# Optimization experiments

Measured on AMD Instinct MI355X. Metric: run time of the kernel, lower is better.

The kernel has to match this reference:

```python
import jax, jax.numpy as jnp
import numpy as np

N = 100000
E = 1600000
NFEAT = 256
NCLASS = 40
H1, C1 = 8, 8  # layer1: 8 heads x 8 channels, concat -> 64
EPS = 1e-16
NEG_SLOPE = 0.2


def setup_inputs() -> dict:
    key = jax.random.key(0)
    ks = jax.random.split(key, 10)
    x = jax.random.normal(ks[0], (N, NFEAT), dtype=jnp.float32)
    # random edges with no self-loops (PyG GATConv removes then re-adds self loops)
    src = jax.random.randint(ks[1], (E,), 0, N)
    off = jax.random.randint(ks[2], (E,), 1, N)
    dst = (src + off) % N
    edge_index = jnp.stack([src, dst]).astype(jnp.int64)
    glorot = lambda k, shp, fan: jax.random.uniform(k, shp, jnp.float32, -1.0, 1.0) * np.sqrt(6.0 / fan)
    # layer 1: in=256 -> heads=8, out=8
    W1 = glorot(ks[3], (NFEAT, H1 * C1), NFEAT + H1 * C1)
    att_src1 = glorot(ks[4], (H1, C1), 2 * C1)
    att_dst1 = glorot(ks[5], (H1, C1), 2 * C1)
    b1 = jnp.zeros((H1 * C1,), jnp.float32)
    # layer 2: in=64 -> heads=1, out=nclass
    W2 = glorot(ks[6], (H1 * C1, NCLASS), H1 * C1 + NCLASS)
    att_src2 = glorot(ks[7], (1, NCLASS), 2 * NCLASS)
    att_dst2 = glorot(ks[8], (1, NCLASS), 2 * NCLASS)
    b2 = jnp.zeros((NCLASS,), jnp.float32)
    return {"x": x, "edge_index": edge_index, "W1": W1, "att_src1": att_src1,
            "att_dst1": att_dst1, "b1": b1, "W2": W2, "att_src2": att_src2,
            "att_dst2": att_dst2, "b2": b2}


def gat_conv(x, src, dst, W, att_src, att_dst, bias, heads, out_ch):
    n = x.shape[0]
    h = (x @ W).reshape(n, heads, out_ch)               # [N,H,C]
    a_src = (h * att_src[None]).sum(-1)                  # [N,H]
    a_dst = (h * att_dst[None]).sum(-1)                  # [N,H]
    e = jax.nn.leaky_relu(a_src[src] + a_dst[dst], NEG_SLOPE)  # [E,H]
    # segment softmax over incoming edges of each target node
    m = jax.ops.segment_max(e, dst, num_segments=n)
    e = jnp.exp(e - m[dst])
    s = jax.ops.segment_sum(e, dst, num_segments=n)
    alpha = e / (s[dst] + EPS)                           # [E,H]
    msg = h[src] * alpha[..., None]                      # [E,H,C]
    out = jax.ops.segment_sum(msg, dst, num_segments=n)  # [N,H,C]
    return out.reshape(n, heads * out_ch) + bias


def reference(x, edge_index, W1, att_src1, att_dst1, b1, W2, att_src2, att_dst2, b2):
    # add self loops (PyG GATConv default add_self_loops=True)
    loops = jnp.arange(N, dtype=edge_index.dtype)
    src = jnp.concatenate([edge_index[0], loops])
    dst = jnp.concatenate([edge_index[1], loops])
    h = gat_conv(x, src, dst, W1, att_src1, att_dst1, b1, H1, C1)  # [N,64]
    h = jax.nn.elu(h)
    out = gat_conv(h, src, dst, W2, att_src2, att_dst2, b2, 1, NCLASS)  # [N,nclass]
    return out
```

## Files before the change

### kernel.cpp

```cpp
#include <hip/hip_runtime.h>
#include <hip/hip_bf16.h>

#define NN 100000
#define NE 1600000
#define NF 256
#define NC 40
#define NH 8
#define D1 64
#define NEG 0.2f
#define BSHIFT 7
#define BSZ 128
#define NB ((NN + BSZ - 1) / BSZ)
#define EPB 4096
#define NBLK ((NE + EPB - 1) / EPB)

typedef __attribute__((ext_vector_type(8))) short short8;
typedef __attribute__((ext_vector_type(4))) float f32x4;

static __device__ __forceinline__ float lrelu(float x) { return x > 0.f ? x : NEG * x; }

static __device__ __forceinline__ float2 bfx2(unsigned u) {
    union { unsigned q; float f; } a, b;
    a.q = u << 16;
    b.q = u & 0xFFFF0000u;
    return make_float2(a.f, b.f);
}

static __device__ __forceinline__ unsigned packbf2(float x, float y) {
    unsigned xu = __float_as_uint(x), yu = __float_as_uint(y);
    xu = (xu + 0x7FFFu + ((xu >> 16) & 1u)) >> 16;
    yu = (yu + 0x7FFFu + ((yu >> 16) & 1u)) >> 16;
    return xu | (yu << 16);
}

static __device__ __forceinline__ unsigned short f2b(float x) {
    unsigned u = __float_as_uint(x);
    u = (u + 0x7FFFu + ((u >> 16) & 1u)) >> 16;
    return (unsigned short)u;
}


__launch_bounds__(256)
__global__ void bhist_k(const int* __restrict__ dst, int* __restrict__ cnt) {
    __shared__ int hist[NB];
    int i = blockIdx.x, t = threadIdx.x;
    for (int b = t; b < NB; b += 256) hist[b] = 0;
    __syncthreads();
    int e0 = i * EPB;
    #pragma unroll
    for (int k = 0; k < EPB / 256; ++k) {
        int e = e0 + k * 256 + t;
        if (e < NE) atomicAdd(&hist[dst[e] >> BSHIFT], 1);
    }
    __syncthreads();
    for (int b = t; b < NB; b += 256) cnt[i * NB + b] = hist[b];
}

__launch_bounds__(256)
__global__ void bscan2_k(int* __restrict__ cnt, int* __restrict__ btot) {
    __shared__ int ps[256];
    int b = blockIdx.x, t = threadIdx.x;
    int i0 = 2 * t;
    int a = (i0 < NBLK) ? cnt[i0 * NB + b] : 0;
    int c = (i0 + 1 < NBLK) ? cnt[(i0 + 1) * NB + b] : 0;
    int s = a + c;
    ps[t] = s;
    __syncthreads();
    #pragma unroll
    for (int off = 1; off < 256; off <<= 1) {
        int x = (t >= off) ? ps[t - off] : 0;
        __syncthreads();
        ps[t] += x;
        __syncthreads();
    }
    int ex = ps[t] - s;
    if (i0 < NBLK) cnt[i0 * NB + b] = ex;
    if (i0 + 1 < NBLK) cnt[(i0 + 1) * NB + b] = ex + a;
    if (t == 255) btot[b] = ps[255];
}

__launch_bounds__(256)
__global__ void bscanB_k(const int* __restrict__ btot, int* __restrict__ bbase) {
    __shared__ int ps[256];
    int t = threadIdx.x;
    int j0 = 4 * t;
    int v[4]; int s = 0;
    #pragma unroll
    for (int k = 0; k < 4; ++k) { v[k] = (j0 + k < NB) ? btot[j0 + k] : 0; s += v[k]; }
    ps[t] = s;
    __syncthreads();
    #pragma unroll
    for (int off = 1; off < 256; off <<= 1) {
        int x = (t >= off) ? ps[t - off] : 0;
        __syncthreads();
        ps[t] += x;
        __syncthreads();
    }
    int run = ps[t] - s;
    #pragma unroll
    for (int k = 0; k < 4; ++k) { if (j0 + k < NB) bbase[j0 + k] = run; run += v[k]; }
    if (t == 0) bbase[NB] = NE;
}

__launch_bounds__(256)
__global__ void bplace_k(const int* __restrict__ src, const int* __restrict__ dst,
                         const int* __restrict__ cnt, const int* __restrict__ bbase,
                         long long* __restrict__ tmp) {
    __shared__ int loff[NB];
    int i = blockIdx.x, t = threadIdx.x;
    for (int b = t; b < NB; b += 256) loff[b] = bbase[b] + cnt[i * NB + b];
    __syncthreads();
    int e0 = i * EPB;
    #pragma unroll
    for (int k = 0; k < EPB / 256; ++k) {
        int e = e0 + k * 256 + t;
        if (e < NE) {
            int d = dst[e];
            int p = atomicAdd(&loff[d >> BSHIFT], 1);
            tmp[p] = ((long long)d << 32) | (unsigned)src[e];
        }
    }
}

__launch_bounds__(256)
__global__ void scatter2_k(const long long* __restrict__ tmp, const int* __restrict__ bbase,
                           int* __restrict__ rowptr, int* __restrict__ col) {
    __shared__ int lcnt[BSZ];
    __shared__ int lrow[BSZ];
    __shared__ int ls[BSZ];
    int b = blockIdx.x, t = threadIdx.x;
    int n0 = b << BSHIFT;
    if (t < BSZ) lcnt[t] = 0;
    __syncthreads();
    int beg = bbase[b], end = bbase[b + 1];
    for (int p = beg + t; p < end; p += 256) {
        int d = (int)(tmp[p] >> 32);
        atomicAdd(&lcnt[d - n0], 1);
    }
    __syncthreads();
    if (t < BSZ) ls[t] = lcnt[t];
    __syncthreads();
    #pragma unroll
    for (int off = 1; off < BSZ; off <<= 1) {
        int x = 0;
        if (t < BSZ && t >= off) x = ls[t - off];
        __syncthreads();
        if (t < BSZ) ls[t] += x;
        __syncthreads();
    }
    if (t < BSZ) {
        int ex = ls[t] - lcnt[t];
        lrow[t] = beg + ex;
        if (n0 + t < NN) rowptr[n0 + t] = beg + ex;
        lcnt[t] = 0;
    }
    if (b == NB - 1 && t == 0) rowptr[NN] = NE;
    __syncthreads();
    for (int p = beg + t; p < end; p += 256) {
        long long v = tmp[p];
        int d = (int)(v >> 32);
        int s = (int)(v & 0xFFFFFFFFLL);
        int o = atomicAdd(&lcnt[d - n0], 1);
        col[lrow[d - n0] + o] = s;
    }
}


__launch_bounds__(256)
__global__ void gemm1_k(const float* __restrict__ x, const float* __restrict__ W,
                        unsigned short* __restrict__ h1b) {
    __shared__ unsigned short wsw[8 * 4 * 64 * 8];
    int tid = threadIdx.x;
    int wid = tid >> 6, lane = tid & 63;
    int r0 = blockIdx.x * 128 + wid * 32;

    #pragma unroll
    for (int it = 0; it < 16; ++it) {
        int idx4 = it * 256 + tid;
        int k = idx4 >> 4;
        int c0 = (idx4 & 15) * 4;
        float4 v = *(const float4*)&W[k * 64 + c0];
        int kt = k >> 5, kg = (k >> 3) & 3, kr = k & 7;
        float vv[4] = {v.x, v.y, v.z, v.w};
        #pragma unroll
        for (int j = 0; j < 4; ++j) {
            int c = c0 + j;
            int dest = (((kt * 4 + (c >> 4)) * 64) + kg * 16 + (c & 15)) * 8 + kr;
            wsw[dest] = f2b(vv[j]);
        }
    }
    __syncthreads();

    int arow0 = r0 + (lane & 15);
    int kg8 = (lane >> 4) * 8;
    f32x4 acc[2][4] = {};
    for (int kt = 0; kt < 8; ++kt) {
        short8 af[2];
        #pragma unroll
        for (int rt = 0; rt < 2; ++rt) {
            int row = arow0 + rt * 16;
            float4 v0 = make_float4(0.f, 0.f, 0.f, 0.f), v1 = v0;
            if (row < NN) {
                const float* px = &x[row * NF + kt * 32 + kg8];
                v0 = *(const float4*)px;
                v1 = *(const float4*)(px + 4);
            }
            unsigned p0 = packbf2(v0.x, v0.y), p1 = packbf2(v0.z, v0.w);
            unsigned p2 = packbf2(v1.x, v1.y), p3 = packbf2(v1.z, v1.w);
            af[rt][0] = (short)(p0 & 0xFFFF); af[rt][1] = (short)(p0 >> 16);
            af[rt][2] = (short)(p1 & 0xFFFF); af[rt][3] = (short)(p1 >> 16);
            af[rt][4] = (short)(p2 & 0xFFFF); af[rt][5] = (short)(p2 >> 16);
            af[rt][6] = (short)(p3 & 0xFFFF); af[rt][7] = (short)(p3 >> 16);
        }
        #pragma unroll
        for (int ct = 0; ct < 4; ++ct) {
            short8 bf = *(const short8*)&wsw[((kt * 4 + ct) * 64 + lane) * 8];
            acc[0][ct] = __builtin_amdgcn_mfma_f32_16x16x32_bf16(af[0], bf, acc[0][ct], 0, 0, 0);
            acc[1][ct] = __builtin_amdgcn_mfma_f32_16x16x32_bf16(af[1], bf, acc[1][ct], 0, 0, 0);
        }
    }

    int ccol = lane & 15;
    int crow0 = r0 + (lane >> 4) * 4;
    #pragma unroll
    for (int rt = 0; rt < 2; ++rt) {
        #pragma unroll
        for (int r = 0; r < 4; ++r) {
            int grow = crow0 + rt * 16 + r;
            if (grow < NN) {
                #pragma unroll
                for (int ct = 0; ct < 4; ++ct)
                    h1b[grow * D1 + ct * 16 + ccol] = f2b(acc[rt][ct][r]);
            }
        }
    }
}


__global__ void attn1_k(const unsigned short* __restrict__ h1b, const float* __restrict__ asrc,
                        const float* __restrict__ adst,
                        float* __restrict__ as1, float* __restrict__ ad1) {
    int t = blockIdx.x * blockDim.x + threadIdx.x;
    if (t >= NN * NH) return;
    int n = t >> 3, h = t & 7;
    uint4 v = *(const uint4*)&h1b[n * D1 + h * 8];
    float hv[8];
    float2 p;
    p = bfx2(v.x); hv[0] = p.x; hv[1] = p.y;
    p = bfx2(v.y); hv[2] = p.x; hv[3] = p.y;
    p = bfx2(v.z); hv[4] = p.x; hv[5] = p.y;
    p = bfx2(v.w); hv[6] = p.x; hv[7] = p.y;
    float sa = 0.f, sd = 0.f;
    #pragma unroll
    for (int c = 0; c < 8; ++c) {
        sa = fmaf(hv[c], asrc[h * 8 + c], sa);
        sd = fmaf(hv[c], adst[h * 8 + c], sd);
    }
    as1[t] = sa;
    ad1[t] = sd;
}


__launch_bounds__(256)
__global__ void agg1_k(const unsigned short* __restrict__ h1b, const float* __restrict__ as1,
                       const float* __restrict__ ad1,
                       const int* __restrict__ rowptr, const int* __restrict__ col,
                       const float* __restrict__ b1, unsigned short* __restrict__ h1outb) {
    int n = blockIdx.x * 4 + (threadIdx.x >> 6);
    if (n >= NN) return;
    int lane = threadIdx.x & 63;
    int g = lane >> 3, ln = lane & 7;
    int row0 = rowptr[n];
    int d = rowptr[n + 1] - row0;
    float adh = ad1[n * 8 + ln];

    float acc[8] = {};
    float wsum = 0.f;
    for (int j = 0; j <= d; j += 8) {
        int jj = j + g;
        int s = (jj < d) ? col[row0 + jj] : n;
        float e = lrelu(as1[s * 8 + ln] + adh);
        float wgt = (jj <= d) ? __expf(e) : 0.f;
        wsum += wgt;
        uint4 hv = *(const uint4*)&h1b[s * D1 + ln * 8];
        float2 p;
        p = bfx2(hv.x); acc[0] = fmaf(p.x, wgt, acc[0]); acc[1] = fmaf(p.y, wgt, acc[1]);
        p = bfx2(hv.y); acc[2] = fmaf(p.x, wgt, acc[2]); acc[3] = fmaf(p.y, wgt, acc[3]);
        p = bfx2(hv.z); acc[4] = fmaf(p.x, wgt, acc[4]); acc[5] = fmaf(p.y, wgt, acc[5]);
        p = bfx2(hv.w); acc[6] = fmaf(p.x, wgt, acc[6]); acc[7] = fmaf(p.y, wgt, acc[7]);
    }
    #pragma unroll
    for (int off = 8; off <= 32; off <<= 1) {
        wsum += __shfl_xor(wsum, off, 64);
        #pragma unroll
        for (int k = 0; k < 8; ++k) acc[k] += __shfl_xor(acc[k], off, 64);
    }
    if (g == 0) {
        float inv = 1.f / (wsum + 1e-16f);
        unsigned u[4];
        #pragma unroll
        for (int k = 0; k < 4; ++k) {
            float v0 = fmaf(acc[2 * k], inv, b1[ln * 8 + 2 * k]);
            float v1 = fmaf(acc[2 * k + 1], inv, b1[ln * 8 + 2 * k + 1]);
            v0 = (v0 > 0.f) ? v0 : (__expf(v0) - 1.f);
            v1 = (v1 > 0.f) ? v1 : (__expf(v1) - 1.f);
            u[k] = packbf2(v0, v1);
        }
        uint4 w = {u[0], u[1], u[2], u[3]};
        *(uint4*)&h1outb[n * D1 + ln * 8] = w;
    }
}


__launch_bounds__(256)
__global__ void gemm2_k(const unsigned short* __restrict__ h1outb, const float* __restrict__ W2,
                        float* __restrict__ h2p) {
    __shared__ float xs[64 * 68];
    __shared__ float ws[64 * 40];
    int r0 = blockIdx.x * 64;
    int tid = threadIdx.x;
    #pragma unroll
    for (int it = 0; it < 4; ++it) {
        int idx = tid + it * 256;
        int row = idx >> 4;
        int q = (idx & 15) * 4;
        int gr = r0 + row;
        float f0 = 0.f, f1 = 0.f, f2 = 0.f, f3 = 0.f;
        if (gr < NN) {
            uint2 v = *(const uint2*)&h1outb[gr * D1 + q];
            float2 p0 = bfx2(v.x), p1 = bfx2(v.y);
            f0 = p0.x; f1 = p0.y; f2 = p1.x; f3 = p1.y;
        }
        xs[row * 68 + q] = f0;
        xs[row * 68 + q + 1] = f1;
        xs[row * 68 + q + 2] = f2;
        xs[row * 68 + q + 3] = f3;
    }
    #pragma unroll
    for (int it = 0; it < 10; ++it) {
        int idx = tid + it * 256;
        if (idx < 64 * 40) ws[idx] = W2[idx];
    }
    __syncthreads();
    int r = tid >> 2, q = tid & 3;
    float acc[10] = {};
    #pragma unroll 4
    for (int k = 0; k < 64; ++k) {
        float xv = xs[r * 68 + k];
        #pragma unroll
        for (int i = 0; i < 10; ++i)
            acc[i] = fmaf(xv, ws[k * 40 + q * 10 + i], acc[i]);
    }
    int gr = r0 + r;
    if (gr < NN) {
        #pragma unroll
        for (int i = 0; i < 10; ++i) h2p[gr * 64 + q * 10 + i] = acc[i];
    }
    for (int idx = tid; idx < 64 * 24; idx += 256) {
        int row = idx / 24, c = 40 + idx % 24;
        int g2 = r0 + row;
        if (g2 < NN) h2p[g2 * 64 + c] = 0.f;
    }
}


__global__ void attn2_k(const float* __restrict__ h2p, const float* __restrict__ asrc,
                        const float* __restrict__ adst,
                        float* __restrict__ as2, float* __restrict__ ad2) {
    int n = blockIdx.x * blockDim.x + threadIdx.x;
    if (n >= NN) return;
    float sa = 0.f, sd = 0.f;
    #pragma unroll
    for (int c0 = 0; c0 < NC; c0 += 4) {
        float4 v = *(const float4*)&h2p[n * 64 + c0];
        float4 a = *(const float4*)&asrc[c0];
        float4 b = *(const float4*)&adst[c0];
        sa += v.x * a.x + v.y * a.y + v.z * a.z + v.w * a.w;
        sd += v.x * b.x + v.y * b.y + v.z * b.z + v.w * b.w;
    }
    as2[n] = sa;
    ad2[n] = sd;
}


__launch_bounds__(256)
__global__ void agg2_k(const float* __restrict__ h2p, const float* __restrict__ as2,
                       const float* __restrict__ ad2,
                       const int* __restrict__ rowptr, const int* __restrict__ col,
                       const float* __restrict__ b2, float* __restrict__ out) {
    int n = blockIdx.x * 4 + (threadIdx.x >> 6);
    if (n >= NN) return;
    int lane = threadIdx.x & 63;
    int g = lane >> 3, ln = lane & 7;
    int row0 = rowptr[n];
    int d = rowptr[n + 1] - row0;
    float adn = ad2[n];

    float acc[8] = {};
    float wsum = 0.f;
    for (int j = 0; j <= d; j += 8) {
        int jj = j + g;
        int s = (jj < d) ? col[row0 + jj] : n;
        float e = lrelu(as2[s] + adn);
        float wgt = (jj <= d) ? __expf(e) : 0.f;
        wsum += wgt;
        float4 v0 = *(const float4*)&h2p[s * 64 + ln * 8];
        float4 v1 = *(const float4*)&h2p[s * 64 + ln * 8 + 4];
        acc[0] = fmaf(v0.x, wgt, acc[0]); acc[1] = fmaf(v0.y, wgt, acc[1]);
        acc[2] = fmaf(v0.z, wgt, acc[2]); acc[3] = fmaf(v0.w, wgt, acc[3]);
        acc[4] = fmaf(v1.x, wgt, acc[4]); acc[5] = fmaf(v1.y, wgt, acc[5]);
        acc[6] = fmaf(v1.z, wgt, acc[6]); acc[7] = fmaf(v1.w, wgt, acc[7]);
    }
    #pragma unroll
    for (int off = 8; off <= 32; off <<= 1) {
        wsum += __shfl_xor(wsum, off, 64);
        #pragma unroll
        for (int k = 0; k < 8; ++k) acc[k] += __shfl_xor(acc[k], off, 64);
    }
    if (g == 0 && ln < 5) {
        float inv8 = 0.125f / (wsum * 0.125f + 1e-16f);
        float4 o0, o1;
        o0.x = fmaf(acc[0], inv8, b2[ln * 8 + 0]);
        o0.y = fmaf(acc[1], inv8, b2[ln * 8 + 1]);
        o0.z = fmaf(acc[2], inv8, b2[ln * 8 + 2]);
        o0.w = fmaf(acc[3], inv8, b2[ln * 8 + 3]);
        o1.x = fmaf(acc[4], inv8, b2[ln * 8 + 4]);
        o1.y = fmaf(acc[5], inv8, b2[ln * 8 + 5]);
        o1.z = fmaf(acc[6], inv8, b2[ln * 8 + 6]);
        o1.w = fmaf(acc[7], inv8, b2[ln * 8 + 7]);
        *(float4*)&out[n * NC + ln * 8] = o0;
        *(float4*)&out[n * NC + ln * 8 + 4] = o1;
    }
}


extern "C" void kernel_launch(void* const* d_in, const int* in_sizes, int n_in,
                              void* d_out, int out_size, void* d_ws, size_t ws_size,
                              hipStream_t stream) {
    const float* x = (const float*)d_in[0];
    const int* ei = (const int*)d_in[1];
    const int* src = ei;
    const int* dst = ei + NE;
    const float* W1 = (const float*)d_in[2];
    const float* asrc1 = (const float*)d_in[3];
    const float* adst1 = (const float*)d_in[4];
    const float* b1 = (const float*)d_in[5];
    const float* W2 = (const float*)d_in[6];
    const float* asrc2 = (const float*)d_in[7];
    const float* adst2 = (const float*)d_in[8];
    const float* b2 = (const float*)d_in[9];
    float* out = (float*)d_out;

    char* ws = (char*)d_ws;
    unsigned short* h1b    = (unsigned short*)(ws + 0);
    float*          as1    = (float*)(ws + 12800000);
    float*          ad1    = (float*)(ws + 16000000);
    float*          h2p    = (float*)(ws + 0);
    unsigned short* h1outb = (unsigned short*)(ws + 25600000);
    long long*      tmp    = (long long*)(ws + 25600000);
    float*          as2    = (float*)(ws + 38400000);
    float*          ad2    = (float*)(ws + 38800000);
    int*            col    = (int*)(ws + 39200000);
    int*            cnt    = (int*)(ws + 39200000);
    int*            rowptr = (int*)(ws + 45600000);
    int*            btot   = (int*)(ws + 46000128);
    int*            bbase  = (int*)(ws + 46003264);

    bhist_k<<<NBLK, 256, 0, stream>>>(dst, cnt);
    bscan2_k<<<NB, 256, 0, stream>>>(cnt, btot);
    bscanB_k<<<1, 256, 0, stream>>>(btot, bbase);
    bplace_k<<<NBLK, 256, 0, stream>>>(src, dst, cnt, bbase, tmp);
    scatter2_k<<<NB, 256, 0, stream>>>(tmp, bbase, rowptr, col);

    gemm1_k<<<(NN + 127) / 128, 256, 0, stream>>>(x, W1, h1b);
    attn1_k<<<(NN * NH + 255) / 256, 256, 0, stream>>>(h1b, asrc1, adst1, as1, ad1);
    agg1_k<<<(NN + 3) / 4, 256, 0, stream>>>(h1b, as1, ad1, rowptr, col, b1, h1outb);

    gemm2_k<<<(NN + 63) / 64, 256, 0, stream>>>(h1outb, W2, h2p);
    attn2_k<<<(NN + 255) / 256, 256, 0, stream>>>(h2p, asrc2, adst2, as2, ad2);
    agg2_k<<<(NN + 3) / 4, 256, 0, stream>>>(h2p, as2, ad2, rowptr, col, b2, out);
}
```

Measured before the change: 230.3 us.

## Reorder layer-2 GAT to aggregate before the linear projection

Because the linear projection commutes with the weighted sum, layer 2 now aggregates the 64-wide bf16 hidden features first and applies W2 and the bias afterwards. The attention logits are computed directly from the hidden features using W2·att vectors precomputed per block. This removes the fp32 h2p intermediate (64 floats per node, padded from 40) and makes the edge gather read 128 bytes of bf16 per neighbour instead of 256 bytes of fp32. In exchange the aggregated result is rounded to bf16 before the final GEMM, which adds some precision loss.

```diff
diff --git a/kernel.cpp b/kernel.cpp
--- a/kernel.cpp
+++ b/kernel.cpp
@@ -313,70 +313,40 @@
 
 
 __launch_bounds__(256)
-__global__ void gemm2_k(const unsigned short* __restrict__ h1outb, const float* __restrict__ W2,
-                        float* __restrict__ h2p) {
-    __shared__ float xs[64 * 68];
-    __shared__ float ws[64 * 40];
-    int r0 = blockIdx.x * 64;
+__global__ void attn2_k(const unsigned short* __restrict__ h1outb, const float* __restrict__ W2,
+                        const float* __restrict__ asrc, const float* __restrict__ adst,
+                        float* __restrict__ as2, float* __restrict__ ad2) {
+    __shared__ float w2a[64], w2d[64];
     int tid = threadIdx.x;
-    #pragma unroll
-    for (int it = 0; it < 4; ++it) {
-        int idx = tid + it * 256;
-        int row = idx >> 4;
-        int q = (idx & 15) * 4;
-        int gr = r0 + row;
-        float f0 = 0.f, f1 = 0.f, f2 = 0.f, f3 = 0.f;
-        if (gr < NN) {
-            uint2 v = *(const uint2*)&h1outb[gr * D1 + q];
-            float2 p0 = bfx2(v.x), p1 = bfx2(v.y);
-            f0 = p0.x; f1 = p0.y; f2 = p1.x; f3 = p1.y;
-        }
-        xs[row * 68 + q] = f0;
-        xs[row * 68 + q + 1] = f1;
-        xs[row * 68 + q + 2] = f2;
-        xs[row * 68 + q + 3] = f3;
-    }
-    #pragma unroll
-    for (int it = 0; it < 10; ++it) {
-        int idx = tid + it * 256;
-        if (idx < 64 * 40) ws[idx] = W2[idx];
-    }
-    __syncthreads();
-    int r = tid >> 2, q = tid & 3;
-    float acc[10] = {};
-    #pragma unroll 4
-    for (int k = 0; k < 64; ++k) {
-        float xv = xs[r * 68 + k];
-        #pragma unroll
-        for (int i = 0; i < 10; ++i)
-            acc[i] = fmaf(xv, ws[k * 40 + q * 10 + i], acc[i]);
-    }
-    int gr = r0 + r;
-    if (gr < NN) {
-        #pragma unroll
-        for (int i = 0; i < 10; ++i) h2p[gr * 64 + q * 10 + i] = acc[i];
-    }
-    for (int idx = tid; idx < 64 * 24; idx += 256) {
-        int row = idx / 24, c = 40 + idx % 24;
-        int g2 = r0 + row;
-        if (g2 < NN) h2p[g2 * 64 + c] = 0.f;
-    }
-}
-
-
-__global__ void attn2_k(const float* __restrict__ h2p, const float* __restrict__ asrc,
-                        const float* __restrict__ adst,
-                        float* __restrict__ as2, float* __restrict__ ad2) {
-    int n = blockIdx.x * blockDim.x + threadIdx.x;
+    if (tid < 128) {
+        int c = tid & 63;
+        const float* av = (tid < 64) ? asrc : adst;
+        float s = 0.f;
+        #pragma unroll
+        for (int j = 0; j < NC; ++j) s = fmaf(W2[c * NC + j], av[j], s);
+        if (tid < 64) w2a[c] = s; else w2d[c] = s;
+    }
+    __syncthreads();
+    int n = blockIdx.x * 256 + tid;
     if (n >= NN) return;
     float sa = 0.f, sd = 0.f;
     #pragma unroll
-    for (int c0 = 0; c0 < NC; c0 += 4) {
-        float4 v = *(const float4*)&h2p[n * 64 + c0];
-        float4 a = *(const float4*)&asrc[c0];
-        float4 b = *(const float4*)&adst[c0];
-        sa += v.x * a.x + v.y * a.y + v.z * a.z + v.w * a.w;
-        sd += v.x * b.x + v.y * b.y + v.z * b.z + v.w * b.w;
+    for (int q = 0; q < 8; ++q) {
+        uint4 v = *(const uint4*)&h1outb[n * D1 + q * 8];
+        int c0 = q * 8;
+        float2 p;
+        p = bfx2(v.x);
+        sa = fmaf(p.x, w2a[c0], sa);     sd = fmaf(p.x, w2d[c0], sd);
+        sa = fmaf(p.y, w2a[c0 + 1], sa); sd = fmaf(p.y, w2d[c0 + 1], sd);
+        p = bfx2(v.y);
+        sa = fmaf(p.x, w2a[c0 + 2], sa); sd = fmaf(p.x, w2d[c0 + 2], sd);
+        sa = fmaf(p.y, w2a[c0 + 3], sa); sd = fmaf(p.y, w2d[c0 + 3], sd);
+        p = bfx2(v.z);
+        sa = fmaf(p.x, w2a[c0 + 4], sa); sd = fmaf(p.x, w2d[c0 + 4], sd);
+        sa = fmaf(p.y, w2a[c0 + 5], sa); sd = fmaf(p.y, w2d[c0 + 5], sd);
+        p = bfx2(v.w);
+        sa = fmaf(p.x, w2a[c0 + 6], sa); sd = fmaf(p.x, w2d[c0 + 6], sd);
+        sa = fmaf(p.y, w2a[c0 + 7], sa); sd = fmaf(p.y, w2d[c0 + 7], sd);
     }
     as2[n] = sa;
     ad2[n] = sd;
@@ -384,10 +354,10 @@
 
 
 __launch_bounds__(256)
-__global__ void agg2_k(const float* __restrict__ h2p, const float* __restrict__ as2,
+__global__ void agg2_k(const unsigned short* __restrict__ h1outb, const float* __restrict__ as2,
                        const float* __restrict__ ad2,
                        const int* __restrict__ rowptr, const int* __restrict__ col,
-                       const float* __restrict__ b2, float* __restrict__ out) {
+                       unsigned short* __restrict__ zb) {
     int n = blockIdx.x * 4 + (threadIdx.x >> 6);
     if (n >= NN) return;
     int lane = threadIdx.x & 63;
@@ -404,12 +374,12 @@
         float e = lrelu(as2[s] + adn);
         float wgt = (jj <= d) ? __expf(e) : 0.f;
         wsum += wgt;
-        float4 v0 = *(const float4*)&h2p[s * 64 + ln * 8];
-        float4 v1 = *(const float4*)&h2p[s * 64 + ln * 8 + 4];
-        acc[0] = fmaf(v0.x, wgt, acc[0]); acc[1] = fmaf(v0.y, wgt, acc[1]);
-        acc[2] = fmaf(v0.z, wgt, acc[2]); acc[3] = fmaf(v0.w, wgt, acc[3]);
-        acc[4] = fmaf(v1.x, wgt, acc[4]); acc[5] = fmaf(v1.y, wgt, acc[5]);
-        acc[6] = fmaf(v1.z, wgt, acc[6]); acc[7] = fmaf(v1.w, wgt, acc[7]);
+        uint4 hv = *(const uint4*)&h1outb[s * D1 + ln * 8];
+        float2 p;
+        p = bfx2(hv.x); acc[0] = fmaf(p.x, wgt, acc[0]); acc[1] = fmaf(p.y, wgt, acc[1]);
+        p = bfx2(hv.y); acc[2] = fmaf(p.x, wgt, acc[2]); acc[3] = fmaf(p.y, wgt, acc[3]);
+        p = bfx2(hv.z); acc[4] = fmaf(p.x, wgt, acc[4]); acc[5] = fmaf(p.y, wgt, acc[5]);
+        p = bfx2(hv.w); acc[6] = fmaf(p.x, wgt, acc[6]); acc[7] = fmaf(p.y, wgt, acc[7]);
     }
     #pragma unroll
     for (int off = 8; off <= 32; off <<= 1) {
@@ -417,19 +387,63 @@
         #pragma unroll
         for (int k = 0; k < 8; ++k) acc[k] += __shfl_xor(acc[k], off, 64);
     }
-    if (g == 0 && ln < 5) {
-        float inv8 = 0.125f / (wsum * 0.125f + 1e-16f);
-        float4 o0, o1;
-        o0.x = fmaf(acc[0], inv8, b2[ln * 8 + 0]);
-        o0.y = fmaf(acc[1], inv8, b2[ln * 8 + 1]);
-        o0.z = fmaf(acc[2], inv8, b2[ln * 8 + 2]);
-        o0.w = fmaf(acc[3], inv8, b2[ln * 8 + 3]);
-        o1.x = fmaf(acc[4], inv8, b2[ln * 8 + 4]);
-        o1.y = fmaf(acc[5], inv8, b2[ln * 8 + 5]);
-        o1.z = fmaf(acc[6], inv8, b2[ln * 8 + 6]);
-        o1.w = fmaf(acc[7], inv8, b2[ln * 8 + 7]);
-        *(float4*)&out[n * NC + ln * 8] = o0;
-        *(float4*)&out[n * NC + ln * 8 + 4] = o1;
+    if (g == 0) {
+        float inv = 1.f / (wsum + 1e-16f);
+        unsigned u[4];
+        #pragma unroll
+        for (int k = 0; k < 4; ++k)
+            u[k] = packbf2(acc[2 * k] * inv, acc[2 * k + 1] * inv);
+        uint4 w = {u[0], u[1], u[2], u[3]};
+        *(uint4*)&zb[n * D1 + ln * 8] = w;
+    }
+}
+
+
+__launch_bounds__(256)
+__global__ void gemm2_k(const unsigned short* __restrict__ zb, const float* __restrict__ W2,
+                        const float* __restrict__ b2, float* __restrict__ out) {
+    __shared__ float xs[64 * 68];
+    __shared__ float wsm[64 * 40];
+    __shared__ float bs[40];
+    int r0 = blockIdx.x * 64;
+    int tid = threadIdx.x;
+    #pragma unroll
+    for (int it = 0; it < 4; ++it) {
+        int idx = tid + it * 256;
+        int row = idx >> 4;
+        int q = (idx & 15) * 4;
+        int gr = r0 + row;
+        float f0 = 0.f, f1 = 0.f, f2 = 0.f, f3 = 0.f;
+        if (gr < NN) {
+            uint2 v = *(const uint2*)&zb[gr * D1 + q];
+            float2 p0 = bfx2(v.x), p1 = bfx2(v.y);
+            f0 = p0.x; f1 = p0.y; f2 = p1.x; f3 = p1.y;
+        }
+        xs[row * 68 + q] = f0;
+        xs[row * 68 + q + 1] = f1;
+        xs[row * 68 + q + 2] = f2;
+        xs[row * 68 + q + 3] = f3;
+    }
+    #pragma unroll
+    for (int it = 0; it < 10; ++it) {
+        int idx = tid + it * 256;
+        if (idx < 64 * 40) wsm[idx] = W2[idx];
+    }
+    if (tid < 40) bs[tid] = b2[tid];
+    __syncthreads();
+    int r = tid >> 2, q = tid & 3;
+    float acc[10] = {};
+    #pragma unroll 4
+    for (int k = 0; k < 64; ++k) {
+        float xv = xs[r * 68 + k];
+        #pragma unroll
+        for (int i = 0; i < 10; ++i)
+            acc[i] = fmaf(xv, wsm[k * 40 + q * 10 + i], acc[i]);
+    }
+    int gr = r0 + r;
+    if (gr < NN) {
+        #pragma unroll
+        for (int i = 0; i < 10; ++i) out[gr * NC + q * 10 + i] = acc[i] + bs[q * 10 + i];
     }
 }
 
@@ -453,9 +467,9 @@
 
     char* ws = (char*)d_ws;
     unsigned short* h1b    = (unsigned short*)(ws + 0);
+    unsigned short* zb     = (unsigned short*)(ws + 0);
     float*          as1    = (float*)(ws + 12800000);
     float*          ad1    = (float*)(ws + 16000000);
-    float*          h2p    = (float*)(ws + 0);
     unsigned short* h1outb = (unsigned short*)(ws + 25600000);
     long long*      tmp    = (long long*)(ws + 25600000);
     float*          as2    = (float*)(ws + 38400000);
@@ -476,7 +490,7 @@
     attn1_k<<<(NN * NH + 255) / 256, 256, 0, stream>>>(h1b, asrc1, adst1, as1, ad1);
     agg1_k<<<(NN + 3) / 4, 256, 0, stream>>>(h1b, as1, ad1, rowptr, col, b1, h1outb);
 
-    gemm2_k<<<(NN + 63) / 64, 256, 0, stream>>>(h1outb, W2, h2p);
-    attn2_k<<<(NN + 255) / 256, 256, 0, stream>>>(h2p, asrc2, adst2, as2, ad2);
-    agg2_k<<<(NN + 3) / 4, 256, 0, stream>>>(h2p, as2, ad2, rowptr, col, b2, out);
-}
+    attn2_k<<<(NN + 255) / 256, 256, 0, stream>>>(h1outb, W2, asrc2, adst2, as2, ad2);
+    agg2_k<<<(NN + 3) / 4, 256, 0, stream>>>(h1outb, as2, ad2, rowptr, col, zb);
+    gemm2_k<<<(NN + 63) / 64, 256, 0, stream>>>(zb, W2, b2, out);
+}
```

Result: faster. 212.8 us (-7.6%).
